# Performance work log

Hardware: AMD Instinct MI355X
Metric: run time of the kernel (lower is better)

Reference implementation:

```python
import jax, jax.numpy as jnp
import numpy as np

B, T, H = 16384, 96, 256  # batch, history steps, lstm hidden

def _p(k, shape, fan_in):
    return jax.random.normal(k, shape, jnp.float32) / np.float32(np.sqrt(fan_in))

def setup_inputs() -> dict:
    key = jax.random.key(0)
    ks = jax.random.split(key, 16)
    z = lambda n: jnp.zeros((n,), jnp.float32)
    return {
        "spatial_feature": jax.random.normal(ks[0], (B, 1297), jnp.float32),
        "temporal_feature": jax.random.normal(ks[1], (B, T, 56), jnp.float32),
        "sl_w": _p(ks[2], (2, 4), 4),        "sl_b": z(2),
        "st_w": _p(ks[3], (8, 12), 12),      "st_b": z(8),
        "seg_w": _p(ks[4], (512, 1276), 1276), "seg_b": z(512),
        "l1_w": _p(ks[5], (256, 527), 527),  "l1_b": z(256),
        "l2_w": _p(ks[6], (128, 256), 256),  "l2_b": z(128),
        "w_ih": _p(ks[7], (4 * H, 56), 56),  "b_ih": z(4 * H),
        "w_hh": _p(ks[8], (4 * H, H), H),    "b_hh": z(4 * H),
        "l4_w": _p(ks[9], (256, H + 128), H + 128), "l4_b": z(256),
        "l5_w": _p(ks[10], (128, 256), 256), "l5_b": z(128),
        "l6_w": _p(ks[11], (128, 128), 128), "l6_b": z(128),
        "l7_w": _p(ks[12], (1, 128), 128),   "l7_b": z(1),
        "future_preds": 0,
    }

def _lin(x, w, b):
    return x @ w.T + b

def reference(spatial_feature, temporal_feature, sl_w, sl_b, st_w, st_b,
              seg_w, seg_b, l1_w, l1_b, l2_w, l2_b, w_ih, b_ih, w_hh, b_hh,
              l4_w, l4_b, l5_w, l5_b, l6_w, l6_b, l7_w, l7_b, future_preds):
    # spatial embedding chain (computed once)
    out_1 = _lin(spatial_feature[:, 0:4], sl_w, sl_b)
    out_2 = _lin(spatial_feature[:, 4:16], st_w, st_b)
    out_3 = _lin(spatial_feature[:, 16:1292], seg_w, seg_b)
    rest = spatial_feature[:, 1292:]
    out_4 = _lin(jnp.concatenate([out_1, out_2, out_3, rest], axis=1), l1_w, l1_b)
    out_5 = _lin(out_4, l2_w, l2_b)  # [B,128]

    batch = temporal_feature.shape[0]
    h0 = jnp.zeros((batch, H), jnp.float32)
    c0 = jnp.zeros((batch, H), jnp.float32)

    def step(carry, x_t):  # x_t: [B,56]
        h, c = carry
        gates = x_t @ w_ih.T + b_ih + h @ w_hh.T + b_hh  # [B,4H]
        i, f, g, o = jnp.split(gates, 4, axis=1)         # torch gate order i,f,g,o
        c = jax.nn.sigmoid(f) * c + jax.nn.sigmoid(i) * jnp.tanh(g)
        h = jax.nn.sigmoid(o) * jnp.tanh(c)
        return (h, c), None

    (h_t, c_t), _ = jax.lax.scan(step, (h0, c0), jnp.swapaxes(temporal_feature, 0, 1))
    # torch loop computes the MLP every step but only the last output is kept;
    # computing it once on the final h_t is identical math (future_preds == 0).
    x = _lin(jnp.concatenate([out_5, h_t], axis=1), l4_w, l4_b)
    out = _lin(_lin(_lin(x, l5_w, l5_b), l6_w, l6_b), l7_w, l7_b)  # [B,1]
    return out
```

## Files before the change

### kernel.cpp

```cpp
#include <hip/hip_runtime.h>
#include <hip/hip_bf16.h>
#include <math.h>

typedef __bf16 bf16_t;
typedef float  f32x4  __attribute__((ext_vector_type(4)));
typedef unsigned int uint32;
typedef unsigned char uint8;
typedef long long ll_t;
typedef long long ll2 __attribute__((ext_vector_type(2)));

#define WS_WSP    0
#define WS_AH     5248
#define WS_U527   6272
#define WS_BIAS   8384
#define WS_BIASG  8448
#define WS_WC     12544

__device__ __forceinline__ float sigmoid_hw(float x) {
    float e = __builtin_amdgcn_exp2f(-1.44269504f * x);
    return __builtin_amdgcn_rcpf(1.f + e);
}
__device__ __forceinline__ float tanh_hw(float x) {
    float e = __builtin_amdgcn_exp2f(2.88539008f * x);
    return 1.f - 2.f * __builtin_amdgcn_rcpf(1.f + e);
}

__global__ void k_head(const float* __restrict__ sl_w, const float* __restrict__ sl_b,
                       const float* __restrict__ st_w, const float* __restrict__ st_b,
                       const float* __restrict__ seg_b,
                       const float* __restrict__ l1_w, const float* __restrict__ l1_b,
                       const float* __restrict__ l2_w, const float* __restrict__ l2_b,
                       const float* __restrict__ l4_w, const float* __restrict__ l4_b,
                       const float* __restrict__ l5_w, const float* __restrict__ l5_b,
                       const float* __restrict__ l6_w, const float* __restrict__ l6_b,
                       const float* __restrict__ l7_w, const float* __restrict__ l7_b,
                       float* __restrict__ wsp, float* __restrict__ ah,
                       float* __restrict__ u527_out, float* __restrict__ bias_out) {
    __shared__ float v2[128], v3[256], aa[384], u256[256], u527[527];
    __shared__ float red[8];
    const int t = threadIdx.x;

    if (t < 128) { float s = 0.f; for (int i = 0; i < 128; ++i) s += l7_w[i] * l6_w[i*128 + t]; v2[t] = s; }
    __syncthreads();
    if (t < 256) { float s = 0.f; for (int i = 0; i < 128; ++i) s += v2[i] * l5_w[i*256 + t]; v3[t] = s; }
    __syncthreads();
    if (t < 384) { float s = 0.f; for (int i = 0; i < 256; ++i) s += v3[i] * l4_w[i*384 + t]; aa[t] = s; }
    __syncthreads();
    if (t < 256) { float s = 0.f; for (int i = 0; i < 128; ++i) s += aa[i] * l2_w[i*256 + t]; u256[t] = s; }
    if (t < 256) ah[t] = aa[128 + t];
    __syncthreads();
    for (int j = t; j < 527; j += 512) {
        float s = 0.f;
        for (int i = 0; i < 256; ++i) s += u256[i] * l1_w[i*527 + j];
        u527[j] = s; u527_out[j] = s;
    }
    __syncthreads();
    if (t < 4)              { float s = 0.f; for (int i = 0; i < 2; ++i) s += u527[i]     * sl_w[i*4  + t];      wsp[t] = s; }
    else if (t < 16)        { int c = t - 4;  float s = 0.f; for (int i = 0; i < 8; ++i) s += u527[2+i] * st_w[i*12 + c]; wsp[t] = s; }
    else if (t < 21)        { wsp[1292 + (t - 16)] = u527[522 + (t - 16)]; }
    float p = 0.f;
    if (t < 128) p += l7_w[t] * l6_b[t] + v2[t] * l5_b[t] + aa[t] * l2_b[t];
    if (t < 256) p += v3[t] * l4_b[t] + u256[t] * l1_b[t];
    if (t < 2)   p += u527[t] * sl_b[t];
    if (t < 8)   p += u527[2 + t] * st_b[t];
    p += u527[10 + t] * seg_b[t];
    p += __shfl_xor(p, 1);  p += __shfl_xor(p, 2);  p += __shfl_xor(p, 4);
    p += __shfl_xor(p, 8);  p += __shfl_xor(p, 16); p += __shfl_xor(p, 32);
    if ((t & 63) == 0) red[t >> 6] = p;
    __syncthreads();
    if (t == 0) {
        float s = l7_b[0];
        for (int i = 0; i < 8; ++i) s += red[i];
        *bias_out = s;
    }
}

__global__ void k_seg(const float* __restrict__ seg_w, const float* __restrict__ u527,
                      float* __restrict__ wsp) {
    int j = blockIdx.x * 256 + threadIdx.x;
    if (j >= 1276) return;
    float s = 0.f;
    for (int i = 0; i < 512; ++i) s += u527[10 + i] * seg_w[i*1276 + j];
    wsp[16 + j] = s;
}

__global__ void k_wcq(const float* __restrict__ w_ih, const float* __restrict__ b_ih,
                      const float* __restrict__ w_hh, const float* __restrict__ b_hh,
                      uint8* __restrict__ wcq, float* __restrict__ biasg) {
    int idx = blockIdx.x * 256 + threadIdx.x;
    if (idx < 1024) biasg[idx] = b_ih[idx] + b_hh[idx];
    if (idx < 327680) {
        int kk = idx >> 15;
        int r  = idx & 32767;
        int w  = r >> 12;
        int r2 = r & 4095;
        int j  = r2 >> 10;
        int r3 = r2 & 1023;
        int lane = r3 >> 4;
        int b  = r3 & 15;
        int f  = 2*j + (b >> 3);
        int e  = b & 7;
        int ht = f >> 2, q = f & 3;
        int n = q*256 + 32*w + 16*ht + (lane & 15);
        int k = kk*32 + ((lane >> 4) << 3) + e;
        float v = 0.f;
        if (k < 56)       v = w_ih[n*56 + k];
        else if (k >= 64) v = w_hh[n*256 + (k - 64)];
        uint32 pk = __builtin_amdgcn_cvt_pk_fp8_f32(v, 0.f, 0, false);
        wcq[idx] = (uint8)(pk & 0xff);
    }
}

__global__ void k_spatial(const float* __restrict__ sp, const float* __restrict__ wsp,
                          const float* __restrict__ bias, float* __restrict__ out) {
    int row  = blockIdx.x * 4 + (threadIdx.x >> 6);
    int lane = threadIdx.x & 63;
    const float* rp = sp + (size_t)row * 1297;
    float s = 0.f;
    for (int k = lane; k < 1297; k += 64) s += rp[k] * wsp[k];
    s += __shfl_xor(s, 1);  s += __shfl_xor(s, 2);  s += __shfl_xor(s, 4);
    s += __shfl_xor(s, 8);  s += __shfl_xor(s, 16); s += __shfl_xor(s, 32);
    if (lane == 0) out[row] = s + bias[0];
}

__launch_bounds__(512, 2)
__global__ void k_lstm(const float* __restrict__ temporal, const uint8* __restrict__ wcq,
                       const float* __restrict__ biasg, const float* __restrict__ ah,
                       float* __restrict__ out) {
    __shared__ __attribute__((aligned(16))) char  Ring[3 * 32768];
    __shared__ __attribute__((aligned(16))) char  At[64 * 328];
    __shared__ __attribute__((aligned(16))) float Xf[64 * 56];
    __shared__ __attribute__((aligned(16))) char  Xd[2048];

    const int tid  = threadIdx.x;
    const int lane = tid & 63;
    const int w    = tid >> 6;
    const int l15  = lane & 15;
    const int l4q  = lane >> 4;
    const int row0 = blockIdx.x * 64;

    f32x4 bias[2][4];
#pragma unroll
    for (int ht = 0; ht < 2; ++ht)
#pragma unroll
        for (int q = 0; q < 4; ++q)
            bias[ht][q] = *reinterpret_cast<const f32x4*>(biasg + q*256 + 32*w + 16*ht + 4*l4q);
    f32x4 ahv[2];
#pragma unroll
    for (int ht = 0; ht < 2; ++ht)
        ahv[ht] = *reinterpret_cast<const f32x4*>(ah + 32*w + 16*ht + 4*l4q);

    long xo0, xo1;
    {
        int b0 = (2*w + 0)*1024 + lane*16;
        int b1 = (2*w + 1)*1024 + lane*16;
        xo0 = (long)(b0/224)*21504 + (b0 % 224);
        xo1 = (long)(b1/224)*21504 + (b1 % 224);
    }
    const char* xbase = (const char*)(temporal + (size_t)row0 * 5376);

    auto stage_w = [&](int slot, int uu) {
        const uint8* src = wcq + uu*32768 + w*4096 + lane*16;
        char* dst = Ring + slot*32768 + w*4096 + lane*16;
#pragma unroll
        for (int i = 0; i < 4; ++i)
            __builtin_amdgcn_global_load_lds(
                (const __attribute__((address_space(1))) uint32*)(src + i*1024),
                (__attribute__((address_space(3))) uint32*)(dst + i*1024), 16, 0, 0);
    };
    auto stage_x = [&](int tt) {
        if (w < 7) {
            const char* s0 = xbase + xo0 + (size_t)tt*224;
            const char* s1 = xbase + xo1 + (size_t)tt*224;
            float* d0 = Xf + (2*w)*256 + lane*4;
            float* d1 = Xf + (2*w+1)*256 + lane*4;
            __builtin_amdgcn_global_load_lds((const __attribute__((address_space(1))) uint32*)s0,
                                             (__attribute__((address_space(3))) uint32*)d0, 16, 0, 0);
            __builtin_amdgcn_global_load_lds((const __attribute__((address_space(1))) uint32*)s1,
                                             (__attribute__((address_space(3))) uint32*)d1, 16, 0, 0);
        } else {
            const char* s0 = xbase + lane*16;
            __builtin_amdgcn_global_load_lds((const __attribute__((address_space(1))) uint32*)s0,
                                             (__attribute__((address_space(3))) uint32*)(Xd + lane*16), 16, 0, 0);
            __builtin_amdgcn_global_load_lds((const __attribute__((address_space(1))) uint32*)(s0 + 1024),
                                             (__attribute__((address_space(3))) uint32*)(Xd + 1024 + lane*16), 16, 0, 0);
        }
    };
    auto conv_x = [&]() {
        int xr = tid >> 3, xs = tid & 7;
        if (xs < 7) {
            const float* xf = Xf + xr*56 + xs*8;
            f32x4 a = *reinterpret_cast<const f32x4*>(xf);
            f32x4 b = *reinterpret_cast<const f32x4*>(xf + 4);
            uint32 lo = __builtin_amdgcn_cvt_pk_fp8_f32(a[0], a[1], 0, false);
            lo = __builtin_amdgcn_cvt_pk_fp8_f32(a[2], a[3], lo, true);
            uint32 hi = __builtin_amdgcn_cvt_pk_fp8_f32(b[0], b[1], 0, false);
            hi = __builtin_amdgcn_cvt_pk_fp8_f32(b[2], b[3], hi, true);
            uint32* p = reinterpret_cast<uint32*>(At + xr*328 + xs*8);
            p[0] = lo; p[1] = hi;
        } else {
            uint32* p = reinterpret_cast<uint32*>(At + xr*328 + 56);
            p[0] = 0u; p[1] = 0u;
        }
    };

    stage_x(0);
    stage_w(0, 0); stage_w(1, 1);
    for (int i = tid; i < 1312; i += 512)
        *reinterpret_cast<f32x4*>(At + i*16) = (f32x4){0.f,0.f,0.f,0.f};
    asm volatile("s_waitcnt vmcnt(0)" ::: "memory");
    __builtin_amdgcn_s_barrier();
    conv_x();
    asm volatile("s_waitcnt lgkmcnt(0)" ::: "memory");
    __builtin_amdgcn_s_barrier();

    f32x4 cst[4][2];
    f32x4 hv[4][2];
#pragma unroll
    for (int rt = 0; rt < 4; ++rt)
#pragma unroll
        for (int ht = 0; ht < 2; ++ht) cst[rt][ht] = (f32x4){0.f,0.f,0.f,0.f};

    int sl = 0;
#pragma unroll 1
    for (int t = 0; t < 96; ++t) {
        f32x4 acc[4][2][4];
#pragma unroll
        for (int rt = 0; rt < 4; ++rt)
#pragma unroll
            for (int ht = 0; ht < 2; ++ht)
#pragma unroll
                for (int q = 0; q < 4; ++q)
                    acc[rt][ht][q] = bias[ht][q];

#pragma unroll 1
        for (int c = 0; c < 10; ++c) {
            {
                int s2 = sl + 2; if (s2 >= 3) s2 -= 3;
                int u2 = c + 2;  if (u2 >= 10) u2 -= 10;
                stage_w(s2, u2);
            }
            if (c == 0) stage_x(t < 95 ? t + 1 : 95);
            if (c < 3) asm volatile("s_waitcnt vmcnt(10)" ::: "memory");
            else       asm volatile("s_waitcnt vmcnt(8)"  ::: "memory");

            const char* wb = Ring + sl*32768 + w*4096 + lane*16;
            ll_t Af[8];
#pragma unroll
            for (int j = 0; j < 4; ++j) {
                ll2 pr = *reinterpret_cast<const ll2*>(wb + j*1024);
                Af[2*j]   = pr.x;
                Af[2*j+1] = pr.y;
            }
            ll_t Bv[4];
#pragma unroll
            for (int rt = 0; rt < 4; ++rt)
                Bv[rt] = *reinterpret_cast<const ll_t*>(At + (rt*16 + l15)*328 + c*32 + l4q*8);
#pragma unroll
            for (int ht = 0; ht < 2; ++ht)
#pragma unroll
                for (int q = 0; q < 4; ++q) {
                    ll_t A = Af[ht*4 + q];
#pragma unroll
                    for (int rt = 0; rt < 4; ++rt)
                        acc[rt][ht][q] = __builtin_amdgcn_mfma_f32_16x16x32_fp8_fp8(
                            A, Bv[rt], acc[rt][ht][q], 0, 0, 0);
                }
            sl = sl + 1; if (sl >= 3) sl -= 3;
        }

#pragma unroll
        for (int rt = 0; rt < 4; ++rt)
#pragma unroll
            for (int ht = 0; ht < 2; ++ht)
#pragma unroll
                for (int e = 0; e < 4; ++e) {
                    float ig = sigmoid_hw(acc[rt][ht][0][e]);
                    float fg = sigmoid_hw(acc[rt][ht][1][e]);
                    float gt = tanh_hw  (acc[rt][ht][2][e]);
                    float og = sigmoid_hw(acc[rt][ht][3][e]);
                    float cn = fg * cst[rt][ht][e] + ig * gt;
                    cst[rt][ht][e] = cn;
                    hv[rt][ht][e] = og * tanh_hw(cn);
                }

        if (t < 95) {
            __builtin_amdgcn_s_barrier();
#pragma unroll
            for (int rt = 0; rt < 4; ++rt)
#pragma unroll
                for (int ht = 0; ht < 2; ++ht) {
                    uint32 pk = __builtin_amdgcn_cvt_pk_fp8_f32(hv[rt][ht][0], hv[rt][ht][1], 0, false);
                    pk = __builtin_amdgcn_cvt_pk_fp8_f32(hv[rt][ht][2], hv[rt][ht][3], pk, true);
                    *reinterpret_cast<uint32*>(
                        At + (rt*16 + l15)*328 + 64 + 32*w + 16*ht + 4*l4q) = pk;
                }
            conv_x();
            asm volatile("s_waitcnt lgkmcnt(0)" ::: "memory");
            __builtin_amdgcn_s_barrier();
        }
    }

    {
        float part[4];
#pragma unroll
        for (int rt = 0; rt < 4; ++rt) {
            float s = 0.f;
#pragma unroll
            for (int ht = 0; ht < 2; ++ht)
#pragma unroll
                for (int e = 0; e < 4; ++e)
                    s += ahv[ht][e] * hv[rt][ht][e];
            s += __shfl_xor(s, 16);
            s += __shfl_xor(s, 32);
            part[rt] = s;
        }
        __builtin_amdgcn_s_barrier();
        float* sc = reinterpret_cast<float*>(Ring);
        if (l4q == 0)
#pragma unroll
            for (int rt = 0; rt < 4; ++rt)
                sc[w*64 + rt*16 + l15] = part[rt];
        asm volatile("s_waitcnt lgkmcnt(0)" ::: "memory");
        __builtin_amdgcn_s_barrier();
        if (tid < 64) {
            float s = 0.f;
#pragma unroll
            for (int wv = 0; wv < 8; ++wv) s += sc[wv*64 + tid];
            out[row0 + tid] += s;
        }
    }
}

extern "C" void kernel_launch(void* const* d_in, const int* in_sizes, int n_in,
                              void* d_out, int out_size, void* d_ws, size_t ws_size,
                              hipStream_t stream) {
    const float* spatial  = (const float*)d_in[0];
    const float* temporal = (const float*)d_in[1];
    const float* sl_w = (const float*)d_in[2];  const float* sl_b = (const float*)d_in[3];
    const float* st_w = (const float*)d_in[4];  const float* st_b = (const float*)d_in[5];
    const float* seg_w = (const float*)d_in[6]; const float* seg_b = (const float*)d_in[7];
    const float* l1_w = (const float*)d_in[8];  const float* l1_b = (const float*)d_in[9];
    const float* l2_w = (const float*)d_in[10]; const float* l2_b = (const float*)d_in[11];
    const float* w_ih = (const float*)d_in[12]; const float* b_ih = (const float*)d_in[13];
    const float* w_hh = (const float*)d_in[14]; const float* b_hh = (const float*)d_in[15];
    const float* l4_w = (const float*)d_in[16]; const float* l4_b = (const float*)d_in[17];
    const float* l5_w = (const float*)d_in[18]; const float* l5_b = (const float*)d_in[19];
    const float* l6_w = (const float*)d_in[20]; const float* l6_b = (const float*)d_in[21];
    const float* l7_w = (const float*)d_in[22]; const float* l7_b = (const float*)d_in[23];

    char* ws = (char*)d_ws;
    float*  wsp   = (float*)(ws + WS_WSP);
    float*  ah    = (float*)(ws + WS_AH);
    float*  u527  = (float*)(ws + WS_U527);
    float*  biasT = (float*)(ws + WS_BIAS);
    float*  biasg = (float*)(ws + WS_BIASG);
    uint8*  wcq   = (uint8*)(ws + WS_WC);

    float* out = (float*)d_out;

    hipLaunchKernelGGL(k_head, dim3(1), dim3(512), 0, stream,
                       sl_w, sl_b, st_w, st_b, seg_b, l1_w, l1_b, l2_w, l2_b,
                       l4_w, l4_b, l5_w, l5_b, l6_w, l6_b, l7_w, l7_b,
                       wsp, ah, u527, biasT);
    hipLaunchKernelGGL(k_seg, dim3(5), dim3(256), 0, stream, seg_w, u527, wsp);
    hipLaunchKernelGGL(k_wcq, dim3(1280), dim3(256), 0, stream,
                       w_ih, b_ih, w_hh, b_hh, wcq, biasg);
    hipLaunchKernelGGL(k_spatial, dim3(16384/4), dim3(256), 0, stream,
                       spatial, wsp, biasT, out);
    hipLaunchKernelGGL(k_lstm, dim3(256), dim3(512), 0, stream,
                       temporal, wcq, biasg, ah, out);
}
```

Measured before the change: 1.192 ms.

## Double-buffer LSTM activations with swizzled LDS layout and deeper weight prefetch

Splits the padded activation tile into separate double-buffered x and h buffers using an XOR-swizzled layout instead of a padded row stride. This lets the pre-write barrier at each timestep be dropped. Weight staging moves to after the MFMAs with a prefetch distance of three slots, filling the whole ring up front, and vmcnt waits are retuned. The aim is fewer barriers and bank conflicts and more load/compute overlap, at the cost of more LDS and fragile waitcnt accounting.

```diff
diff --git a/kernel.cpp b/kernel.cpp
--- a/kernel.cpp
+++ b/kernel.cpp
@@ -128,7 +128,8 @@
                        const float* __restrict__ biasg, const float* __restrict__ ah,
                        float* __restrict__ out) {
     __shared__ __attribute__((aligned(16))) char  Ring[3 * 32768];
-    __shared__ __attribute__((aligned(16))) char  At[64 * 328];
+    __shared__ __attribute__((aligned(16))) char  Ah[2 * 16384];
+    __shared__ __attribute__((aligned(16))) char  Xa[2 * 4096];
     __shared__ __attribute__((aligned(16))) float Xf[64 * 56];
     __shared__ __attribute__((aligned(16))) char  Xd[2048];
 
@@ -150,6 +151,15 @@
     for (int ht = 0; ht < 2; ++ht)
         ahv[ht] = *reinterpret_cast<const f32x4*>(ah + 32*w + 16*ht + 4*l4q);
 
+    int hbase[4], hswz[4], xbase_o[4];
+#pragma unroll
+    for (int rt = 0; rt < 4; ++rt) {
+        int row = rt*16 + l15;
+        hswz[rt]   = row & 7;
+        hbase[rt]  = row*256 + (l4q << 3);
+        xbase_o[rt]= row*64;
+    }
+
     long xo0, xo1;
     {
         int b0 = (2*w + 0)*1024 + lane*16;
@@ -157,7 +167,7 @@
         xo0 = (long)(b0/224)*21504 + (b0 % 224);
         xo1 = (long)(b1/224)*21504 + (b1 % 224);
     }
-    const char* xbase = (const char*)(temporal + (size_t)row0 * 5376);
+    const char* xsrc = (const char*)(temporal + (size_t)row0 * 5376);
 
     auto stage_w = [&](int slot, int uu) {
         const uint8* src = wcq + uu*32768 + w*4096 + lane*16;
@@ -170,8 +180,8 @@
     };
     auto stage_x = [&](int tt) {
         if (w < 7) {
-            const char* s0 = xbase + xo0 + (size_t)tt*224;
-            const char* s1 = xbase + xo1 + (size_t)tt*224;
+            const char* s0 = xsrc + xo0 + (size_t)tt*224;
+            const char* s1 = xsrc + xo1 + (size_t)tt*224;
             float* d0 = Xf + (2*w)*256 + lane*4;
             float* d1 = Xf + (2*w+1)*256 + lane*4;
             __builtin_amdgcn_global_load_lds((const __attribute__((address_space(1))) uint32*)s0,
@@ -179,38 +189,36 @@
             __builtin_amdgcn_global_load_lds((const __attribute__((address_space(1))) uint32*)s1,
                                              (__attribute__((address_space(3))) uint32*)d1, 16, 0, 0);
         } else {
-            const char* s0 = xbase + lane*16;
+            const char* s0 = xsrc + lane*16;
             __builtin_amdgcn_global_load_lds((const __attribute__((address_space(1))) uint32*)s0,
                                              (__attribute__((address_space(3))) uint32*)(Xd + lane*16), 16, 0, 0);
             __builtin_amdgcn_global_load_lds((const __attribute__((address_space(1))) uint32*)(s0 + 1024),
                                              (__attribute__((address_space(3))) uint32*)(Xd + 1024 + lane*16), 16, 0, 0);
         }
     };
-    auto conv_x = [&]() {
+    auto conv_x = [&](int buf) {
         int xr = tid >> 3, xs = tid & 7;
+        uint32 lo = 0u, hi = 0u;
         if (xs < 7) {
             const float* xf = Xf + xr*56 + xs*8;
             f32x4 a = *reinterpret_cast<const f32x4*>(xf);
             f32x4 b = *reinterpret_cast<const f32x4*>(xf + 4);
-            uint32 lo = __builtin_amdgcn_cvt_pk_fp8_f32(a[0], a[1], 0, false);
+            lo = __builtin_amdgcn_cvt_pk_fp8_f32(a[0], a[1], 0, false);
             lo = __builtin_amdgcn_cvt_pk_fp8_f32(a[2], a[3], lo, true);
-            uint32 hi = __builtin_amdgcn_cvt_pk_fp8_f32(b[0], b[1], 0, false);
+            hi = __builtin_amdgcn_cvt_pk_fp8_f32(b[0], b[1], 0, false);
             hi = __builtin_amdgcn_cvt_pk_fp8_f32(b[2], b[3], hi, true);
-            uint32* p = reinterpret_cast<uint32*>(At + xr*328 + xs*8);
-            p[0] = lo; p[1] = hi;
-        } else {
-            uint32* p = reinterpret_cast<uint32*>(At + xr*328 + 56);
-            p[0] = 0u; p[1] = 0u;
-        }
+        }
+        uint32* p = reinterpret_cast<uint32*>(Xa + buf*4096 + xr*64 + ((xs ^ (xr & 7)) << 3));
+        p[0] = lo; p[1] = hi;
     };
 
     stage_x(0);
-    stage_w(0, 0); stage_w(1, 1);
-    for (int i = tid; i < 1312; i += 512)
-        *reinterpret_cast<f32x4*>(At + i*16) = (f32x4){0.f,0.f,0.f,0.f};
+    stage_w(0, 0); stage_w(1, 1); stage_w(2, 2);
+    for (int i = tid; i < 4096; i += 512)
+        reinterpret_cast<uint32*>(Ah)[i] = 0u;
     asm volatile("s_waitcnt vmcnt(0)" ::: "memory");
     __builtin_amdgcn_s_barrier();
-    conv_x();
+    conv_x(0);
     asm volatile("s_waitcnt lgkmcnt(0)" ::: "memory");
     __builtin_amdgcn_s_barrier();
 
@@ -224,6 +232,7 @@
     int sl = 0;
 #pragma unroll 1
     for (int t = 0; t < 96; ++t) {
+        const int par = t & 1, nxt = par ^ 1;
         f32x4 acc[4][2][4];
 #pragma unroll
         for (int rt = 0; rt < 4; ++rt)
@@ -235,14 +244,8 @@
 
 #pragma unroll 1
         for (int c = 0; c < 10; ++c) {
-            {
-                int s2 = sl + 2; if (s2 >= 3) s2 -= 3;
-                int u2 = c + 2;  if (u2 >= 10) u2 -= 10;
-                stage_w(s2, u2);
-            }
-            if (c == 0) stage_x(t < 95 ? t + 1 : 95);
-            if (c < 3) asm volatile("s_waitcnt vmcnt(10)" ::: "memory");
-            else       asm volatile("s_waitcnt vmcnt(8)"  ::: "memory");
+            if (c >= 1 && c <= 3) asm volatile("s_waitcnt vmcnt(10)" ::: "memory");
+            else                  asm volatile("s_waitcnt vmcnt(8)"  ::: "memory");
 
             const char* wb = Ring + sl*32768 + w*4096 + lane*16;
             ll_t Af[8];
@@ -253,9 +256,17 @@
                 Af[2*j+1] = pr.y;
             }
             ll_t Bv[4];
-#pragma unroll
-            for (int rt = 0; rt < 4; ++rt)
-                Bv[rt] = *reinterpret_cast<const ll_t*>(At + (rt*16 + l15)*328 + c*32 + l4q*8);
+            if (c < 2) {
+#pragma unroll
+                for (int rt = 0; rt < 4; ++rt)
+                    Bv[rt] = *reinterpret_cast<const ll_t*>(
+                        Xa + par*4096 + xbase_o[rt] + (((c*4 + l4q) ^ hswz[rt]) << 3));
+            } else {
+#pragma unroll
+                for (int rt = 0; rt < 4; ++rt)
+                    Bv[rt] = *reinterpret_cast<const ll_t*>(
+                        Ah + par*16384 + hbase[rt] + (((c-2) ^ hswz[rt]) << 5));
+            }
 #pragma unroll
             for (int ht = 0; ht < 2; ++ht)
 #pragma unroll
@@ -266,6 +277,11 @@
                         acc[rt][ht][q] = __builtin_amdgcn_mfma_f32_16x16x32_fp8_fp8(
                             A, Bv[rt], acc[rt][ht][q], 0, 0, 0);
                 }
+            {
+                int u3 = c + 3; if (u3 >= 10) u3 -= 10;
+                stage_w(sl, u3);
+            }
+            if (c == 0) stage_x(t < 95 ? t + 1 : 95);
             sl = sl + 1; if (sl >= 3) sl -= 3;
         }
 
@@ -285,17 +301,19 @@
                 }
 
         if (t < 95) {
-            __builtin_amdgcn_s_barrier();
 #pragma unroll
             for (int rt = 0; rt < 4; ++rt)
 #pragma unroll
                 for (int ht = 0; ht < 2; ++ht) {
                     uint32 pk = __builtin_amdgcn_cvt_pk_fp8_f32(hv[rt][ht][0], hv[rt][ht][1], 0, false);
                     pk = __builtin_amdgcn_cvt_pk_fp8_f32(hv[rt][ht][2], hv[rt][ht][3], pk, true);
+                    int row = rt*16 + l15;
+                    int g   = 4*w + 2*ht + (l4q >> 1);
                     *reinterpret_cast<uint32*>(
-                        At + (rt*16 + l15)*328 + 64 + 32*w + 16*ht + 4*l4q) = pk;
+                        Ah + nxt*16384 + row*256 + ((g ^ ((row & 7) << 2)) << 3) + 4*(l4q & 1)) = pk;
                 }
-            conv_x();
+            asm volatile("s_waitcnt vmcnt(12)" ::: "memory");
+            conv_x(nxt);
             asm volatile("s_waitcnt lgkmcnt(0)" ::: "memory");
             __builtin_amdgcn_s_barrier();
         }
@@ -316,6 +334,7 @@
             part[rt] = s;
         }
         __builtin_amdgcn_s_barrier();
+        asm volatile("s_waitcnt vmcnt(0)" ::: "memory");
         float* sc = reinterpret_cast<float*>(Ring);
         if (l4q == 0)
 #pragma unroll
```

After: 1.157 ms, median of 2. 1.03x faster.
